# Kernel optimization log

Measured on AMD Instinct MI355X. Metric: run time of the kernel, lower is better.

The kernel has to match this reference:

```python
import jax, jax.numpy as jnp
import numpy as np

IN_C, OUT_C, K, STRIDE, PAD = 128, 256, 3, 1, 1
B, H, W = 32, 56, 56


def setup_inputs() -> dict:
    key = jax.random.key(0)
    kx, kw = jax.random.split(key)
    x = jax.random.normal(kx, (B, IN_C, H, W), dtype=jnp.float32)
    # He init, matching torch.randn(out_c,in_c,k,k) * (2/(in_c*k*k))**0.5
    Wk = jax.random.normal(kw, (OUT_C, IN_C, K, K), dtype=jnp.float32) * (2.0 / (IN_C * K * K)) ** 0.5
    b = jnp.zeros((OUT_C,), dtype=jnp.float32)
    return {"x": x, "Wk": Wk, "b": b}


def reference(x, Wk, b):
    # Same math as the module's zero-pad + im2col + GEMM pipeline,
    # expressed as a direct convolution (implicit GEMM).
    out = jax.lax.conv_general_dilated(
        x, Wk,
        window_strides=(STRIDE, STRIDE),
        padding=[(PAD, PAD), (PAD, PAD)],
        dimension_numbers=("NCHW", "OIHW", "NCHW"),
    )
    return out + b[None, :, None, None]
```

## Files before the change

### kernel.cpp

```cpp
#include <hip/hip_runtime.h>
#include <hip/hip_bf16.h>

#define IN_C  128
#define OUT_C 256
#define HIMG  56
#define WIMG  56
#define BIMG  32
#define HW    (HIMG * WIMG)
#define KW    1152

#define BM    128
#define TH    4
#define NLOC  224
#define XROWS 6
#define XCOLS 58
#define NPIXT (XROWS * XCOLS)
#define LDK   40

typedef __attribute__((ext_vector_type(8))) short short8;
typedef __attribute__((ext_vector_type(4))) float float4_;

__device__ __forceinline__ unsigned short f32_to_bf16_rne(float f) {
    unsigned u = __builtin_bit_cast(unsigned, f);
    u += 0x7FFFu + ((u >> 16) & 1u);
    return (unsigned short)(u >> 16);
}

__global__ void repack_w(const float* __restrict__ Wk, unsigned short* __restrict__ Wt) {
    int idx = blockIdx.x * 256 + threadIdx.x;
    if (idx >= OUT_C * KW) return;
    int oc  = idx / KW;
    int rem = idx - oc * KW;
    int r   = rem >> 7;
    int ic  = rem & 127;
    Wt[idx] = f32_to_bf16_rne(Wk[oc * KW + ic * 9 + r]);
}

__global__ __launch_bounds__(256, 2) void conv_gemm(
    const float* __restrict__ x, const unsigned short* __restrict__ Wt,
    const float* __restrict__ bias, float* __restrict__ out)
{
    __shared__ short As[BM * LDK];
    __shared__ short Xs[NPIXT * 32];

    const int tid  = threadIdx.x;
    const int lane = tid & 63;
    const int wid  = tid >> 6;
    const int bx   = blockIdx.x;
    const int b    = bx / 14;
    const int h0   = (bx - b * 14) * TH;
    const int oc0  = blockIdx.y * BM;

    const int wm = (wid >> 1) * 64;
    const int wn = (wid & 1) * 112;

    int lp0[7], outoff[7];
    #pragma unroll
    for (int ni = 0; ni < 7; ++ni) {
        int nl  = wn + ni * 16 + (lane & 15);
        int ht_ = nl / 56;
        int wt_ = nl - ht_ * 56;
        lp0[ni]    = (ht_ + 1) * XCOLS + (wt_ + 1);
        outoff[ni] = (h0 + ht_) * WIMG + wt_;
    }

    const short* aptr[4];
    #pragma unroll
    for (int mi = 0; mi < 4; ++mi)
        aptr[mi] = &As[(wm + mi * 16 + (lane & 15)) * LDK + (lane >> 4) * 8];

    float4_ acc[4][7];
    #pragma unroll
    for (int mi = 0; mi < 4; ++mi)
        #pragma unroll
        for (int ni = 0; ni < 7; ++ni) acc[mi][ni] = (float4_)0.0f;

    const int am = tid >> 1, ako = (tid & 1) * 16;
    const int q  = lane >> 4;

    short8 w0, w1;
    {
        const unsigned short* srcA = Wt + (size_t)(oc0 + am) * KW + 0 * 128 + 0 * 32 + ako;
        w0 = *(const short8*)srcA;
        w1 = *(const short8*)(srcA + 8);
    }

    for (int t = 0; t < 36; ++t) {
        const int icq = t / 9;
        const int r   = t - icq * 9;

        if (r == 0) {
            for (int pix = tid; pix < NPIXT; pix += 256) {
                int row  = pix / XCOLS;
                int colw = pix - row * XCOLS;
                int h = h0 + row - 1;
                int w = colw - 1;
                bool valid = ((unsigned)h < HIMG) & ((unsigned)w < WIMG);
                const int sw = (pix >> 1) & 3;
                #pragma unroll
                for (int qb = 0; qb < 4; ++qb) {
                    const float* src = x + (size_t)(b * IN_C + icq * 32 + qb * 8) * HW
                                         + (ptrdiff_t)(h * WIMG + w);
                    short8 v;
                    #pragma unroll
                    for (int j = 0; j < 8; ++j) {
                        float f = valid ? src[(size_t)j * HW] : 0.0f;
                        v[j] = (short)f32_to_bf16_rne(f);
                    }
                    *(short8*)&Xs[pix * 32 + (qb ^ sw) * 8] = v;
                }
            }
        }

        *(short8*)&As[am * LDK + ako]     = w0;
        *(short8*)&As[am * LDK + ako + 8] = w1;
        if (t < 35) {
            const int t1   = t + 1;
            const int icq1 = t1 / 9;
            const int r1   = t1 - icq1 * 9;
            const unsigned short* srcA =
                Wt + (size_t)(oc0 + am) * KW + r1 * 128 + icq1 * 32 + ako;
            w0 = *(const short8*)srcA;
            w1 = *(const short8*)(srcA + 8);
        }
        __syncthreads();

        const int doff = (r / 3 - 1) * XCOLS + (r - (r / 3) * 3 - 1);
        short8 afr[4], bfr[7];
        #pragma unroll
        for (int mi = 0; mi < 4; ++mi) afr[mi] = *(const short8*)aptr[mi];
        #pragma unroll
        for (int ni = 0; ni < 7; ++ni) {
            int lp   = lp0[ni] + doff;
            int slot = q ^ ((lp >> 1) & 3);
            bfr[ni]  = *(const short8*)&Xs[lp * 32 + slot * 8];
        }
        #pragma unroll
        for (int mi = 0; mi < 4; ++mi)
            #pragma unroll
            for (int ni = 0; ni < 7; ++ni)
                acc[mi][ni] = __builtin_amdgcn_mfma_f32_16x16x32_bf16(
                    afr[mi], bfr[ni], acc[mi][ni], 0, 0, 0);
        __syncthreads();
    }

    const int rowg = (lane >> 4) * 4;
    #pragma unroll
    for (int mi = 0; mi < 4; ++mi) {
        #pragma unroll
        for (int v = 0; v < 4; ++v) {
            const int oc = oc0 + wm + mi * 16 + rowg + v;
            const float bv = bias[oc];
            float* obase = out + (size_t)(b * OUT_C + oc) * HW;
            #pragma unroll
            for (int ni = 0; ni < 7; ++ni)
                obase[outoff[ni]] = acc[mi][ni][v] + bv;
        }
    }
}

extern "C" void kernel_launch(void* const* d_in, const int* in_sizes, int n_in,
                              void* d_out, int out_size, void* d_ws, size_t ws_size,
                              hipStream_t stream) {
    const float* x    = (const float*)d_in[0];
    const float* Wk   = (const float*)d_in[1];
    const float* bias = (const float*)d_in[2];
    float* out        = (float*)d_out;
    unsigned short* Wt = (unsigned short*)d_ws;

    repack_w<<<dim3((OUT_C * KW + 255) / 256), dim3(256), 0, stream>>>(Wk, Wt);
    conv_gemm<<<dim3(BIMG * (HIMG / TH), OUT_C / BM), dim3(256), 0, stream>>>(x, Wt, bias, out);
}
```

Before: 214.6 us.

## Load weight fragments directly from global into registers, drop LDS staging and per-step barriers

Removes the shared-memory staging buffer for the weight tile. Each lane now reads its MFMA A-fragments straight from global memory (register prefetch one step ahead). This lets the two barriers per K-step be replaced by barriers only around the input-tile refill every 9 steps, cutting LDS traffic and synchronisation. In exchange there are more redundant global/L2 loads of weights, since warps sharing rows each fetch them, and uncoalesced 16-byte reads strided by KW.

Result: slower. 229.3 us (+6.8%).

```diff
diff --git a/kernel.cpp b/kernel.cpp
--- a/kernel.cpp
+++ b/kernel.cpp
@@ -11,11 +11,9 @@
 
 #define BM    128
 #define TH    4
-#define NLOC  224
 #define XROWS 6
 #define XCOLS 58
 #define NPIXT (XROWS * XCOLS)
-#define LDK   40
 
 typedef __attribute__((ext_vector_type(8))) short short8;
 typedef __attribute__((ext_vector_type(4))) float float4_;
@@ -40,7 +38,6 @@
     const float* __restrict__ x, const unsigned short* __restrict__ Wt,
     const float* __restrict__ bias, float* __restrict__ out)
 {
-    __shared__ short As[BM * LDK];
     __shared__ short Xs[NPIXT * 32];
 
     const int tid  = threadIdx.x;
@@ -64,10 +61,7 @@
         outoff[ni] = (h0 + ht_) * WIMG + wt_;
     }
 
-    const short* aptr[4];
-    #pragma unroll
-    for (int mi = 0; mi < 4; ++mi)
-        aptr[mi] = &As[(wm + mi * 16 + (lane & 15)) * LDK + (lane >> 4) * 8];
+    const unsigned short* aLane = Wt + (size_t)(oc0 + wm + (lane & 15)) * KW + (lane >> 4) * 8;
 
     float4_ acc[4][7];
     #pragma unroll
@@ -75,21 +69,19 @@
         #pragma unroll
         for (int ni = 0; ni < 7; ++ni) acc[mi][ni] = (float4_)0.0f;
 
-    const int am = tid >> 1, ako = (tid & 1) * 16;
-    const int q  = lane >> 4;
+    const int q = lane >> 4;
 
-    short8 w0, w1;
-    {
-        const unsigned short* srcA = Wt + (size_t)(oc0 + am) * KW + 0 * 128 + 0 * 32 + ako;
-        w0 = *(const short8*)srcA;
-        w1 = *(const short8*)(srcA + 8);
-    }
+    short8 anx[4];
+    #pragma unroll
+    for (int mi = 0; mi < 4; ++mi)
+        anx[mi] = *(const short8*)(aLane + (size_t)mi * 16 * KW);
 
     for (int t = 0; t < 36; ++t) {
         const int icq = t / 9;
         const int r   = t - icq * 9;
 
         if (r == 0) {
+            if (t) __syncthreads();
             for (int pix = tid; pix < NPIXT; pix += 256) {
                 int row  = pix / XCOLS;
                 int colw = pix - row * XCOLS;
@@ -110,25 +102,24 @@
                     *(short8*)&Xs[pix * 32 + (qb ^ sw) * 8] = v;
                 }
             }
+            __syncthreads();
         }
 
-        *(short8*)&As[am * LDK + ako]     = w0;
-        *(short8*)&As[am * LDK + ako + 8] = w1;
+        short8 afr[4];
+        #pragma unroll
+        for (int mi = 0; mi < 4; ++mi) afr[mi] = anx[mi];
         if (t < 35) {
             const int t1   = t + 1;
             const int icq1 = t1 / 9;
             const int r1   = t1 - icq1 * 9;
-            const unsigned short* srcA =
-                Wt + (size_t)(oc0 + am) * KW + r1 * 128 + icq1 * 32 + ako;
-            w0 = *(const short8*)srcA;
-            w1 = *(const short8*)(srcA + 8);
+            const int koff = r1 * 128 + icq1 * 32;
+            #pragma unroll
+            for (int mi = 0; mi < 4; ++mi)
+                anx[mi] = *(const short8*)(aLane + (size_t)mi * 16 * KW + koff);
         }
-        __syncthreads();
 
         const int doff = (r / 3 - 1) * XCOLS + (r - (r / 3) * 3 - 1);
-        short8 afr[4], bfr[7];
-        #pragma unroll
-        for (int mi = 0; mi < 4; ++mi) afr[mi] = *(const short8*)aptr[mi];
+        short8 bfr[7];
         #pragma unroll
         for (int ni = 0; ni < 7; ++ni) {
             int lp   = lp0[ni] + doff;
@@ -141,7 +132,6 @@
             for (int ni = 0; ni < 7; ++ni)
                 acc[mi][ni] = __builtin_amdgcn_mfma_f32_16x16x32_bf16(
                     afr[mi], bfr[ni], acc[mi][ni], 0, 0, 0);
-        __syncthreads();
     }
 
     const int rowg = (lane >> 4) * 4;
```
